# Optimization experiments

Hardware: AMD Instinct MI355X
Metric: run time of the kernel (lower is better)

The kernel has to match this reference:

```python
import jax, jax.numpy as jnp
import numpy as np

V, E, H, B, S, O, L = 50257, 256, 512, 64, 1024, 1, 2


def setup_inputs() -> dict:
    key = jax.random.key(0)
    ks = jax.random.split(key, 16)
    s = 0.02
    d = {
        "tokens": jax.random.randint(ks[0], (B, S), 0, V),
        "emb": jax.random.normal(ks[1], (V, E), jnp.float32) * s,
        "fc_w": jax.random.normal(ks[2], (O, H), jnp.float32) * s,
        "fc_b": jnp.zeros((O,), jnp.float32),
    }
    ins = [E, H]
    for l in range(L):
        i = ins[l]
        d[f"gate_w{l}"] = jax.random.normal(ks[3 + 4 * l], (2 * H, i + H), jnp.float32) * s
        d[f"gate_b{l}"] = jnp.zeros((2 * H,), jnp.float32)
        d[f"gi_w{l}"] = jax.random.normal(ks[4 + 4 * l], (H, i), jnp.float32) * s
        d[f"gi_b{l}"] = jnp.zeros((H,), jnp.float32)
        d[f"gh_w{l}"] = jax.random.normal(ks[5 + 4 * l], (H, H), jnp.float32) * s
        d[f"gh_b{l}"] = jnp.zeros((H,), jnp.float32)
    return d


def _cell(x, h, gw, gb, giw, gib, ghw, ghb):
    # gates from concat(input, hidden): [B, 2H]
    gates = jnp.concatenate([x, h], axis=-1) @ gw.T + gb
    r, z = jnp.split(gates, 2, axis=-1)
    r = jax.nn.sigmoid(r)
    z = jax.nn.sigmoid(z)
    n = jnp.tanh(x @ giw.T + gib + r * (h @ ghw.T + ghb))
    return (1.0 - z) * n + z * h  # dropout is identity at inference


def _forward(tokens, emb, fc_w, fc_b, layers):
    x = emb[tokens]  # [B, S, E]
    b = tokens.shape[0]
    h0 = tuple(jnp.zeros((b, H), x.dtype) for _ in layers)

    def step(hs, xt):  # xt: [B, E]
        new = []
        inp = xt
        for h, p in zip(hs, layers):
            h = _cell(inp, h, *p)
            new.append(h)
            inp = h
        return tuple(new), None

    hs, _ = jax.lax.scan(step, h0, jnp.swapaxes(x, 0, 1))  # scan over S
    out = hs[-1] @ fc_w.T + fc_b  # [B, 1]
    return jax.nn.sigmoid(jnp.squeeze(out))  # [B]


def reference(tokens, emb, fc_w, fc_b,
              gate_w0, gate_b0, gi_w0, gi_b0, gh_w0, gh_b0,
              gate_w1, gate_b1, gi_w1, gi_b1, gh_w1, gh_b1):
    layers = [
        (gate_w0, gate_b0, gi_w0, gi_b0, gh_w0, gh_b0),
        (gate_w1, gate_b1, gi_w1, gi_b1, gh_w1, gh_b1),
    ]
    return _forward(tokens, emb, fc_w, fc_b, layers)
```

## Files before the change

kernel.cpp:

```cpp
#include <hip/hip_runtime.h>

typedef _Float16 f16;
typedef _Float16 f16x8 __attribute__((ext_vector_type(8)));
typedef float f32x4 __attribute__((ext_vector_type(4)));

#define B_ 64
#define S_ 1024
#define E_ 256
#define H_ 512
#define NG 1536
#define TCH 128
#define NCHUNK (S_/TCH)
#define ROWS_CH (TCH*B_)
#define HS_LD 536

__device__ __forceinline__ float sigm(float x) { return 1.f / (1.f + __expf(-x)); }

__global__ __launch_bounds__(256) void k_embed(const int* __restrict__ tok,
        const float* __restrict__ emb, f16* __restrict__ X, int t0) {
    int idx = blockIdx.x * 256 + threadIdx.x;
    int r = idx >> 6;
    int c4 = (idx & 63) << 2;
    int t = t0 + (r >> 6), b = r & 63;
    int tk = tok[b * S_ + t];
    float4 v = *reinterpret_cast<const float4*>(emb + (size_t)tk * E_ + c4);
    union { f16 h[4]; unsigned long long u; } w;
    w.h[0] = (f16)v.x; w.h[1] = (f16)v.y; w.h[2] = (f16)v.z; w.h[3] = (f16)v.w;
    *reinterpret_cast<unsigned long long*>(X + (size_t)r * E_ + c4) = w.u;
}

__global__ __launch_bounds__(256) void k_packW(const float* __restrict__ gw, int ld, int off,
        const float* __restrict__ g2, f16* __restrict__ W, int KK) {
    int idx = blockIdx.x * 256 + threadIdx.x;
    int per = KK >> 2;
    if (idx >= NG * per) return;
    int row = idx / per;
    int c4 = (idx % per) << 2;
    const float* src = (row < 1024) ? gw + (size_t)row * ld + off + c4
                                    : g2 + (size_t)(row - 1024) * KK + c4;
    float4 v = *reinterpret_cast<const float4*>(src);
    union { f16 h[4]; unsigned long long u; } w;
    w.h[0] = (f16)v.x; w.h[1] = (f16)v.y; w.h[2] = (f16)v.z; w.h[3] = (f16)v.w;
    *reinterpret_cast<unsigned long long*>(W + (size_t)row * KK + c4) = w.u;
}

__global__ __launch_bounds__(256) void k_packBias(const float* __restrict__ gb,
        const float* __restrict__ gib, float* __restrict__ bias) {
    int i = blockIdx.x * 256 + threadIdx.x;
    if (i < 1024) bias[i] = gb[i];
    else if (i < NG) bias[i] = gib[i - 1024];
}

__global__ __launch_bounds__(256) void k_gemm(const f16* __restrict__ A,
        const f16* __restrict__ Bm, const float* __restrict__ bias,
        f16* __restrict__ C, int K) {
    __shared__ f16 As[64][40];
    __shared__ f16 Bs[64][40];
    const int tid = threadIdx.x;
    const int m0 = blockIdx.y << 6, n0 = blockIdx.x << 6;
    const int w = tid >> 6, l = tid & 63;
    const int wr = (w >> 1) << 5, wc = (w & 1) << 5;
    const int srow = tid >> 2, sc8 = (tid & 3) << 3;
    const int fr = l & 15, kl = (l >> 4) << 3;
    f32x4 acc[2][2] = {};
    for (int k0 = 0; k0 < K; k0 += 32) {
        *reinterpret_cast<f16x8*>(&As[srow][sc8]) =
            *reinterpret_cast<const f16x8*>(A + (size_t)(m0 + srow) * K + k0 + sc8);
        *reinterpret_cast<f16x8*>(&Bs[srow][sc8]) =
            *reinterpret_cast<const f16x8*>(Bm + (size_t)(n0 + srow) * K + k0 + sc8);
        __syncthreads();
        f16x8 a0 = *reinterpret_cast<const f16x8*>(&As[wr + fr][kl]);
        f16x8 a1 = *reinterpret_cast<const f16x8*>(&As[wr + 16 + fr][kl]);
        f16x8 b0 = *reinterpret_cast<const f16x8*>(&Bs[wc + fr][kl]);
        f16x8 b1 = *reinterpret_cast<const f16x8*>(&Bs[wc + 16 + fr][kl]);
        acc[0][0] = __builtin_amdgcn_mfma_f32_16x16x32_f16(a0, b0, acc[0][0], 0, 0, 0);
        acc[0][1] = __builtin_amdgcn_mfma_f32_16x16x32_f16(a0, b1, acc[0][1], 0, 0, 0);
        acc[1][0] = __builtin_amdgcn_mfma_f32_16x16x32_f16(a1, b0, acc[1][0], 0, 0, 0);
        acc[1][1] = __builtin_amdgcn_mfma_f32_16x16x32_f16(a1, b1, acc[1][1], 0, 0, 0);
        __syncthreads();
    }
    for (int fm = 0; fm < 2; ++fm)
        for (int fn = 0; fn < 2; ++fn) {
            int col = n0 + wc + (fn << 4) + fr;
            float bv = bias[col];
            for (int j = 0; j < 4; ++j) {
                int rowg = m0 + wr + (fm << 4) + ((l >> 4) << 2) + j;
                C[(size_t)rowg * NG + col] = (f16)(acc[fm][fn][j] + bv);
            }
        }
}

__global__ __launch_bounds__(256) void k_recur3(
        const f16* __restrict__ Wh0p, const f16* __restrict__ Wh1p,
        const f16* __restrict__ Z0, const f16* __restrict__ Z1,
        const float* __restrict__ ghb0, const float* __restrict__ ghb1,
        f16* hb0, f16* hb1, f16* __restrict__ H0out, int* cnt,
        int t00, int n0, int t01, int n1) {
    __shared__ __align__(16) f16 HS[8 * HS_LD];
    __shared__ __align__(16) f16 hx[8][32];
    const int blk = blockIdx.x;
    const int c = blk & 7;
    const int l = (blk >> 3) & 1;
    const int gg = blk >> 4;
    const int nsteps = l ? n1 : n0;
    if (nsteps <= 0) return;
    const int t0 = l ? t01 : t00;
    const f16* __restrict__ Wh = l ? Wh1p : Wh0p;
    const f16* __restrict__ Z  = l ? Z1 : Z0;
    const float* __restrict__ ghb = l ? ghb1 : ghb0;
    f16* hbuf = l ? hb1 : hb0;
    int* mycnt = cnt + ((l * 8 + c) << 5);
    unsigned long long* hb64 = reinterpret_cast<unsigned long long*>(hbuf);

    const int i0 = gg << 5;
    const int tid = threadIdx.x;
    const int w = tid >> 6;
    const int lane = tid & 63;
    const int colb = lane & 15;
    const int bq = lane & 7;
    const int j4 = lane >> 4;
    const int rrow = lane & 15;
    const int ol = rrow >> 2, gate = rrow & 3;

    f16x8 wA[2][16];
    #pragma unroll
    for (int tl = 0; tl < 2; ++tl) {
        const int out = i0 + (w << 3) + (tl << 2) + ol;
        #pragma unroll
        for (int t = 0; t < 16; ++t) {
            f16x8 v{};
            if (gate < 3)
                v = *reinterpret_cast<const f16x8*>(
                        Wh + ((size_t)(gate * H_ + out)) * H_ + (t << 5) + (j4 << 3));
            wA[tl][t] = v;
        }
    }
    const int outA = i0 + (w << 3) + j4;
    const int outB = outA + 4;
    const float gbA = ghb[outA], gbB = ghb[outB];

    for (int sl = 0; sl < nsteps; ++sl) {
        const int s = t0 + sl;
        const int p = s & 1;
        const size_t zrow = ((size_t)sl * 64 + (c << 3) + bq) * NG;
        float zrA = (float)Z[zrow + outA];
        float zzA = (float)Z[zrow + H_ + outA];
        float znA = (float)Z[zrow + 2 * H_ + outA];
        float zrB = (float)Z[zrow + outB];
        float zzB = (float)Z[zrow + H_ + outB];
        float znB = (float)Z[zrow + 2 * H_ + outB];
        if (tid == 0) {
            const int target = s << 4;
            while (__hip_atomic_load(mycnt, __ATOMIC_RELAXED, __HIP_MEMORY_SCOPE_AGENT) < target) {}
        }
        __syncthreads();
        {
            const size_t srcb = ((size_t)p * 64 + (c << 3)) * 128;
            #pragma unroll
            for (int it = 0; it < 4; ++it) {
                int idx = tid + (it << 8);
                int b = idx >> 7, kq = idx & 127;
                unsigned long long v = __hip_atomic_load(hb64 + srcb + (b << 7) + kq,
                        __ATOMIC_RELAXED, __HIP_MEMORY_SCOPE_AGENT);
                *reinterpret_cast<unsigned long long*>(&HS[b * HS_LD + (kq << 2)]) = v;
            }
        }
        __syncthreads();
        f32x4 a00{}, a01{}, a10{}, a11{};
        #pragma unroll
        for (int t = 0; t < 16; ++t) {
            f16x8 bf = *reinterpret_cast<const f16x8*>(&HS[bq * HS_LD + (t << 5) + (j4 << 3)]);
            if (t & 1) {
                a01 = __builtin_amdgcn_mfma_f32_16x16x32_f16(wA[0][t], bf, a01, 0, 0, 0);
                a11 = __builtin_amdgcn_mfma_f32_16x16x32_f16(wA[1][t], bf, a11, 0, 0, 0);
            } else {
                a00 = __builtin_amdgcn_mfma_f32_16x16x32_f16(wA[0][t], bf, a00, 0, 0, 0);
                a10 = __builtin_amdgcn_mfma_f32_16x16x32_f16(wA[1][t], bf, a10, 0, 0, 0);
            }
        }
        f32x4 dA = a00 + a01;
        f32x4 dB = a10 + a11;
        if (colb < 8) {
            float holdA = (float)HS[bq * HS_LD + outA];
            float holdB = (float)HS[bq * HS_LD + outB];
            float rA = sigm(zrA + dA[0]);
            float zA = sigm(zzA + dA[1]);
            float nA = tanhf(znA + rA * (dA[2] + gbA));
            float rB = sigm(zrB + dB[0]);
            float zB = sigm(zzB + dB[1]);
            float nB = tanhf(znB + rB * (dB[2] + gbB));
            hx[bq][(w << 3) + j4]     = (f16)((1.f - zA) * nA + zA * holdA);
            hx[bq][(w << 3) + 4 + j4] = (f16)((1.f - zB) * nB + zB * holdB);
        }
        __syncthreads();
        if (tid < 64) {
            int b = tid >> 3, seg = tid & 7;
            uint2 v = *reinterpret_cast<const uint2*>(&hx[b][seg << 2]);
            size_t dst = ((size_t)(p ^ 1) * 64 + (c << 3) + b) * 128 + (i0 >> 2) + seg;
            __hip_atomic_store(hb64 + dst, __builtin_bit_cast(unsigned long long, v),
                               __ATOMIC_RELAXED, __HIP_MEMORY_SCOPE_AGENT);
            if (l == 0)
                *reinterpret_cast<uint2*>(
                    &H0out[((size_t)sl * 64 + (c << 3) + b) * H_ + i0 + (seg << 2)]) = v;
        }
        __syncthreads();
        if (tid == 0)
            __hip_atomic_fetch_add(mycnt, 1, __ATOMIC_RELAXED, __HIP_MEMORY_SCOPE_AGENT);
    }
}

__global__ __launch_bounds__(64) void k_final(const f16* __restrict__ h,
        const float* __restrict__ fcw, const float* __restrict__ fcb,
        float* __restrict__ out) {
    int b = threadIdx.x;
    float acc = fcb[0];
    for (int k = 0; k < H_; ++k) acc += (float)h[(size_t)b * H_ + k] * fcw[k];
    out[b] = sigm(acc);
}

extern "C" void kernel_launch(void* const* d_in, const int* in_sizes, int n_in,
                              void* d_out, int out_size, void* d_ws, size_t ws_size,
                              hipStream_t stream) {
    (void)in_sizes; (void)n_in; (void)out_size; (void)ws_size;
    const int*   tokens = (const int*)d_in[0];
    const float* emb  = (const float*)d_in[1];
    const float* fc_w = (const float*)d_in[2];
    const float* fc_b = (const float*)d_in[3];
    const float* gw0  = (const float*)d_in[4];
    const float* gb0  = (const float*)d_in[5];
    const float* giw0 = (const float*)d_in[6];
    const float* gib0 = (const float*)d_in[7];
    const float* ghw0 = (const float*)d_in[8];
    const float* ghb0 = (const float*)d_in[9];
    const float* gw1  = (const float*)d_in[10];
    const float* gb1  = (const float*)d_in[11];
    const float* giw1 = (const float*)d_in[12];
    const float* gib1 = (const float*)d_in[13];
    const float* ghw1 = (const float*)d_in[14];
    const float* ghb1 = (const float*)d_in[15];

    char* base = (char*)d_ws;
    size_t off = 0;
    auto carve = [&](size_t bytes) {
        char* p = base + off;
        off = (off + bytes + 255) & ~(size_t)255;
        return p;
    };
    f16*   Wx0   = (f16*)carve((size_t)NG * 256 * 2);
    f16*   Wh0   = (f16*)carve((size_t)NG * 512 * 2);
    f16*   Wx1   = (f16*)carve((size_t)NG * 512 * 2);
    f16*   Wh1   = (f16*)carve((size_t)NG * 512 * 2);
    float* bias0 = (float*)carve(NG * 4);
    float* bias1 = (float*)carve(NG * 4);
    f16*   hbuf0 = (f16*)carve((size_t)2 * B_ * H_ * 2);
    f16*   hbuf1 = (f16*)carve((size_t)2 * B_ * H_ * 2);
    int*   cnt   = (int*)carve((size_t)16 * 32 * 4);
    f16*   Xc    = (f16*)carve((size_t)ROWS_CH * 256 * 2);
    f16*   Zc0   = (f16*)carve((size_t)ROWS_CH * NG * 2);
    f16*   H0c   = (f16*)carve((size_t)ROWS_CH * 512 * 2);
    f16*   Zc1   = (f16*)carve((size_t)ROWS_CH * NG * 2);

    hipMemsetAsync(hbuf0, 0, (size_t)2 * B_ * H_ * 2, stream);
    hipMemsetAsync(hbuf1, 0, (size_t)2 * B_ * H_ * 2, stream);
    hipMemsetAsync(cnt, 0, (size_t)16 * 32 * 4, stream);

    k_packW<<<384, 256, 0, stream>>>(gw0, 768, 0,    giw0, Wx0, 256);
    k_packW<<<768, 256, 0, stream>>>(gw0, 768, 256,  ghw0, Wh0, 512);
    k_packW<<<768, 256, 0, stream>>>(gw1, 1024, 0,   giw1, Wx1, 512);
    k_packW<<<768, 256, 0, stream>>>(gw1, 1024, 512, ghw1, Wh1, 512);
    k_packBias<<<6, 256, 0, stream>>>(gb0, gib0, bias0);
    k_packBias<<<6, 256, 0, stream>>>(gb1, gib1, bias1);

    dim3 gemmGrid(NG / 64, ROWS_CH / 64);
    for (int ch = 0; ch < NCHUNK; ++ch) {
        int t0 = ch * TCH;
        k_embed<<<ROWS_CH * 64 / 256, 256, 0, stream>>>(tokens, emb, Xc, t0);
        k_gemm<<<gemmGrid, 256, 0, stream>>>(Xc, Wx0, bias0, Zc0, 256);
        k_recur3<<<256, 256, 0, stream>>>(Wh0, Wh1, Zc0, Zc1, ghb0, ghb1,
                                          hbuf0, hbuf1, H0c, cnt,
                                          t0, TCH, t0 - TCH, ch ? TCH : 0);
        k_gemm<<<gemmGrid, 256, 0, stream>>>(H0c, Wx1, bias1, Zc1, 512);
    }
    k_recur3<<<256, 256, 0, stream>>>(Wh0, Wh1, Zc0, Zc1, ghb0, ghb1,
                                      hbuf0, hbuf1, H0c, cnt,
                                      0, 0, (NCHUNK - 1) * TCH, TCH);
    k_final<<<1, 64, 0, stream>>>(hbuf1, fc_w, fc_b, (float*)d_out);
}
```

Measured before the change: 3.344 ms.

## Replace counter barrier with step-tagged ring buffer for hidden-state exchange

The recurrent kernel no longer waits on a per-group atomic counter plus two block barriers before reading the previous hidden state. Each 32-bit hidden-state pair is now stored with the step index in its upper 32 bits into a 4-deep ring, and readers poll each word until the tag matches. This removes the counter spin, the fetch-add and one __syncthreads per step, so producer and consumer handshake per data word. In exchange the exchanged data doubles in size, and correctness depends on a ring depth of 4 being enough to prevent overwrite races. The final hidden state is written to a separate buffer for the output layer.

```diff
diff --git a/kernel.cpp b/kernel.cpp
--- a/kernel.cpp
+++ b/kernel.cpp
@@ -3,6 +3,7 @@
 typedef _Float16 f16;
 typedef _Float16 f16x8 __attribute__((ext_vector_type(8)));
 typedef float f32x4 __attribute__((ext_vector_type(4)));
+typedef unsigned long long u64;
 
 #define B_ 64
 #define S_ 1024
@@ -12,9 +13,12 @@
 #define TCH 128
 #define NCHUNK (S_/TCH)
 #define ROWS_CH (TCH*B_)
-#define HS_LD 536
+#define HS_LD 544
 
 __device__ __forceinline__ float sigm(float x) { return 1.f / (1.f + __expf(-x)); }
+
+#define ALOAD(p) __hip_atomic_load((p), __ATOMIC_RELAXED, __HIP_MEMORY_SCOPE_AGENT)
+#define ASTORE(p, v) __hip_atomic_store((p), (v), __ATOMIC_RELAXED, __HIP_MEMORY_SCOPE_AGENT)
 
 __global__ __launch_bounds__(256) void k_embed(const int* __restrict__ tok,
         const float* __restrict__ emb, f16* __restrict__ X, int t0) {
@@ -24,9 +28,9 @@
     int t = t0 + (r >> 6), b = r & 63;
     int tk = tok[b * S_ + t];
     float4 v = *reinterpret_cast<const float4*>(emb + (size_t)tk * E_ + c4);
-    union { f16 h[4]; unsigned long long u; } w;
+    union { f16 h[4]; u64 u; } w;
     w.h[0] = (f16)v.x; w.h[1] = (f16)v.y; w.h[2] = (f16)v.z; w.h[3] = (f16)v.w;
-    *reinterpret_cast<unsigned long long*>(X + (size_t)r * E_ + c4) = w.u;
+    *reinterpret_cast<u64*>(X + (size_t)r * E_ + c4) = w.u;
 }
 
 __global__ __launch_bounds__(256) void k_packW(const float* __restrict__ gw, int ld, int off,
@@ -39,9 +43,9 @@
     const float* src = (row < 1024) ? gw + (size_t)row * ld + off + c4
                                     : g2 + (size_t)(row - 1024) * KK + c4;
     float4 v = *reinterpret_cast<const float4*>(src);
-    union { f16 h[4]; unsigned long long u; } w;
+    union { f16 h[4]; u64 u; } w;
     w.h[0] = (f16)v.x; w.h[1] = (f16)v.y; w.h[2] = (f16)v.z; w.h[3] = (f16)v.w;
-    *reinterpret_cast<unsigned long long*>(W + (size_t)row * KK + c4) = w.u;
+    *reinterpret_cast<u64*>(W + (size_t)row * KK + c4) = w.u;
 }
 
 __global__ __launch_bounds__(256) void k_packBias(const float* __restrict__ gb,
@@ -90,14 +94,14 @@
         }
 }
 
-__global__ __launch_bounds__(256) void k_recur3(
+__global__ __launch_bounds__(256, 1) void k_recur4(
         const f16* __restrict__ Wh0p, const f16* __restrict__ Wh1p,
         const f16* __restrict__ Z0, const f16* __restrict__ Z1,
         const float* __restrict__ ghb0, const float* __restrict__ ghb1,
-        f16* hb0, f16* hb1, f16* __restrict__ H0out, int* cnt,
+        u64* ring0, u64* ring1, f16* __restrict__ H0out, f16* __restrict__ h1out,
         int t00, int n0, int t01, int n1) {
-    __shared__ __align__(16) f16 HS[8 * HS_LD];
-    __shared__ __align__(16) f16 hx[8][32];
+    __shared__ __align__(16) f16 HS[8][HS_LD];
+    __shared__ __align__(16) f16 hx[8][40];
     const int blk = blockIdx.x;
     const int c = blk & 7;
     const int l = (blk >> 3) & 1;
@@ -108,9 +112,7 @@
     const f16* __restrict__ Wh = l ? Wh1p : Wh0p;
     const f16* __restrict__ Z  = l ? Z1 : Z0;
     const float* __restrict__ ghb = l ? ghb1 : ghb0;
-    f16* hbuf = l ? hb1 : hb0;
-    int* mycnt = cnt + ((l * 8 + c) << 5);
-    unsigned long long* hb64 = reinterpret_cast<unsigned long long*>(hbuf);
+    u64* ring = l ? ring1 : ring0;
 
     const int i0 = gg << 5;
     const int tid = threadIdx.x;
@@ -141,7 +143,6 @@
 
     for (int sl = 0; sl < nsteps; ++sl) {
         const int s = t0 + sl;
-        const int p = s & 1;
         const size_t zrow = ((size_t)sl * 64 + (c << 3) + bq) * NG;
         float zrA = (float)Z[zrow + outA];
         float zzA = (float)Z[zrow + H_ + outA];
@@ -149,27 +150,24 @@
         float zrB = (float)Z[zrow + outB];
         float zzB = (float)Z[zrow + H_ + outB];
         float znB = (float)Z[zrow + 2 * H_ + outB];
-        if (tid == 0) {
-            const int target = s << 4;
-            while (__hip_atomic_load(mycnt, __ATOMIC_RELAXED, __HIP_MEMORY_SCOPE_AGENT) < target) {}
-        }
-        __syncthreads();
         {
-            const size_t srcb = ((size_t)p * 64 + (c << 3)) * 128;
+            const u64* src = ring + ((size_t)(s & 3) * 8 + c) * 2048;
+            u64 g[8];
             #pragma unroll
-            for (int it = 0; it < 4; ++it) {
-                int idx = tid + (it << 8);
-                int b = idx >> 7, kq = idx & 127;
-                unsigned long long v = __hip_atomic_load(hb64 + srcb + (b << 7) + kq,
-                        __ATOMIC_RELAXED, __HIP_MEMORY_SCOPE_AGENT);
-                *reinterpret_cast<unsigned long long*>(&HS[b * HS_LD + (kq << 2)]) = v;
+            for (int i = 0; i < 8; ++i) g[i] = ALOAD(src + (i << 8) + tid);
+            #pragma unroll
+            for (int i = 0; i < 8; ++i) {
+                while ((unsigned)(g[i] >> 32) != (unsigned)s)
+                    g[i] = ALOAD(src + (i << 8) + tid);
+                *reinterpret_cast<unsigned*>(
+                    &HS[i][((tid >> 4) << 5) + ((tid & 15) << 1)]) = (unsigned)g[i];
             }
         }
         __syncthreads();
         f32x4 a00{}, a01{}, a10{}, a11{};
         #pragma unroll
         for (int t = 0; t < 16; ++t) {
-            f16x8 bf = *reinterpret_cast<const f16x8*>(&HS[bq * HS_LD + (t << 5) + (j4 << 3)]);
+            f16x8 bf = *reinterpret_cast<const f16x8*>(&HS[bq][(t << 5) + (j4 << 3)]);
             if (t & 1) {
                 a01 = __builtin_amdgcn_mfma_f32_16x16x32_f16(wA[0][t], bf, a01, 0, 0, 0);
                 a11 = __builtin_amdgcn_mfma_f32_16x16x32_f16(wA[1][t], bf, a11, 0, 0, 0);
@@ -181,8 +179,8 @@
         f32x4 dA = a00 + a01;
         f32x4 dB = a10 + a11;
         if (colb < 8) {
-            float holdA = (float)HS[bq * HS_LD + outA];
-            float holdB = (float)HS[bq * HS_LD + outB];
+            float holdA = (float)HS[bq][outA];
+            float holdB = (float)HS[bq][outB];
             float rA = sigm(zrA + dA[0]);
             float zA = sigm(zzA + dA[1]);
             float nA = tanhf(znA + rA * (dA[2] + gbA));
@@ -193,19 +191,20 @@
             hx[bq][(w << 3) + 4 + j4] = (f16)((1.f - zB) * nB + zB * holdB);
         }
         __syncthreads();
-        if (tid < 64) {
-            int b = tid >> 3, seg = tid & 7;
-            uint2 v = *reinterpret_cast<const uint2*>(&hx[b][seg << 2]);
-            size_t dst = ((size_t)(p ^ 1) * 64 + (c << 3) + b) * 128 + (i0 >> 2) + seg;
-            __hip_atomic_store(hb64 + dst, __builtin_bit_cast(unsigned long long, v),
-                               __ATOMIC_RELAXED, __HIP_MEMORY_SCOPE_AGENT);
+        if (tid < 128) {
+            const int b = tid >> 4, d = tid & 15;
+            unsigned dval = *reinterpret_cast<const unsigned*>(&hx[b][d << 1]);
+            u64 gr = ((u64)(unsigned)(s + 1) << 32) | (u64)dval;
+            ASTORE(ring + ((size_t)((s + 1) & 3) * 8 + c) * 2048
+                        + ((size_t)b << 8) + (gg << 4) + d, gr);
             if (l == 0)
-                *reinterpret_cast<uint2*>(
-                    &H0out[((size_t)sl * 64 + (c << 3) + b) * H_ + i0 + (seg << 2)]) = v;
-        }
-        __syncthreads();
-        if (tid == 0)
-            __hip_atomic_fetch_add(mycnt, 1, __ATOMIC_RELAXED, __HIP_MEMORY_SCOPE_AGENT);
+                *reinterpret_cast<unsigned*>(
+                    &H0out[((size_t)sl * 64 + (c << 3) + b) * H_ + i0 + (d << 1)]) = dval;
+            else if (s == S_ - 1)
+                *reinterpret_cast<unsigned*>(
+                    &h1out[((size_t)(c << 3) + b) * H_ + i0 + (d << 1)]) = dval;
+        }
+        __syncthreads();
     }
 }
 
@@ -252,17 +251,16 @@
     f16*   Wh1   = (f16*)carve((size_t)NG * 512 * 2);
     float* bias0 = (float*)carve(NG * 4);
     float* bias1 = (float*)carve(NG * 4);
-    f16*   hbuf0 = (f16*)carve((size_t)2 * B_ * H_ * 2);
-    f16*   hbuf1 = (f16*)carve((size_t)2 * B_ * H_ * 2);
-    int*   cnt   = (int*)carve((size_t)16 * 32 * 4);
+    u64*   ring0 = (u64*)carve((size_t)4 * 8 * 2048 * 8);
+    u64*   ring1 = (u64*)carve((size_t)4 * 8 * 2048 * 8);
+    f16*   h1out = (f16*)carve((size_t)B_ * H_ * 2);
     f16*   Xc    = (f16*)carve((size_t)ROWS_CH * 256 * 2);
     f16*   Zc0   = (f16*)carve((size_t)ROWS_CH * NG * 2);
     f16*   H0c   = (f16*)carve((size_t)ROWS_CH * 512 * 2);
     f16*   Zc1   = (f16*)carve((size_t)ROWS_CH * NG * 2);
 
-    hipMemsetAsync(hbuf0, 0, (size_t)2 * B_ * H_ * 2, stream);
-    hipMemsetAsync(hbuf1, 0, (size_t)2 * B_ * H_ * 2, stream);
-    hipMemsetAsync(cnt, 0, (size_t)16 * 32 * 4, stream);
+    hipMemsetAsync(ring0, 0, (size_t)4 * 8 * 2048 * 8, stream);
+    hipMemsetAsync(ring1, 0, (size_t)4 * 8 * 2048 * 8, stream);
 
     k_packW<<<384, 256, 0, stream>>>(gw0, 768, 0,    giw0, Wx0, 256);
     k_packW<<<768, 256, 0, stream>>>(gw0, 768, 256,  ghw0, Wh0, 512);
@@ -276,13 +274,13 @@
         int t0 = ch * TCH;
         k_embed<<<ROWS_CH * 64 / 256, 256, 0, stream>>>(tokens, emb, Xc, t0);
         k_gemm<<<gemmGrid, 256, 0, stream>>>(Xc, Wx0, bias0, Zc0, 256);
-        k_recur3<<<256, 256, 0, stream>>>(Wh0, Wh1, Zc0, Zc1, ghb0, ghb1,
-                                          hbuf0, hbuf1, H0c, cnt,
+        k_recur4<<<256, 256, 0, stream>>>(Wh0, Wh1, Zc0, Zc1, ghb0, ghb1,
+                                          ring0, ring1, H0c, h1out,
                                           t0, TCH, t0 - TCH, ch ? TCH : 0);
         k_gemm<<<gemmGrid, 256, 0, stream>>>(H0c, Wx1, bias1, Zc1, 512);
     }
-    k_recur3<<<256, 256, 0, stream>>>(Wh0, Wh1, Zc0, Zc1, ghb0, ghb1,
-                                      hbuf0, hbuf1, H0c, cnt,
+    k_recur4<<<256, 256, 0, stream>>>(Wh0, Wh1, Zc0, Zc1, ghb0, ghb1,
+                                      ring0, ring1, H0c, h1out,
                                       0, 0, (NCHUNK - 1) * TCH, TCH);
-    k_final<<<1, 64, 0, stream>>>(hbuf1, fc_w, fc_b, (float*)d_out);
-}
+    k_final<<<1, 64, 0, stream>>>(h1out, fc_w, fc_b, (float*)d_out);
+}
```

New measurement: 3.143 ms. 6.0% less time.
